# Performance work log

Measured on AMD Instinct MI355X. Metric: run time of the kernel, lower is better.

Reference implementation:

```python
import jax, jax.numpy as jnp
import numpy as np

# TISA RBF basis (helpers l2_dist / rbf_basis in the repo): f_i(d) = a_i * exp(-|b_i| * (d - c_i)^2)

def setup_inputs() -> dict:
    key = jax.random.key(0)
    k = jax.random.split(key, 8)
    B, L, H, D, S, F = 2, 2048, 8, 64, 2, 5
    qs = jax.random.normal(k[0], (B, L, H, D), dtype=jnp.float32)
    ks = jax.random.normal(k[1], (B, L, H, D), dtype=jnp.float32)
    vs = jax.random.normal(k[2], (B, L, H, D), dtype=jnp.float32)
    qs_s = jax.random.uniform(k[3], (B, L, S), dtype=jnp.float32)
    ks_s = jax.random.uniform(k[4], (B, L, S), dtype=jnp.float32)
    a = jax.random.uniform(k[5], (H * F,), dtype=jnp.float32)
    b = jax.random.uniform(k[6], (H * F,), dtype=jnp.float32)
    c = jax.random.normal(k[7], (H * F,), dtype=jnp.float32) * 0.5
    return {"qs": qs, "ks": ks, "vs": vs, "qs_s": qs_s, "ks_s": ks_s, "a": a, "b": b, "c": c}


def _tisa_attention(qs, ks, vs, qs_s, ks_s, a, b, c):
    B, Q, H, D = qs.shape
    F = a.size // H
    aH, bH, cH = (p.reshape(H, F) for p in (a, b, c))
    # pairwise euclidean distance between query and key locations: [B, Q, K]
    diff = qs_s[:, :, None, :] - ks_s[:, None, :, :]
    d = jnp.sqrt(jnp.sum(diff * diff, axis=-1))
    d_ = d[:, None]  # [B, 1, Q, K] broadcast over heads
    # RBF bias summed over F basis functions (small fixed F -> python sum avoids B,H,F,Q,K blowup)
    bias = sum(
        aH[:, f][None, :, None, None]
        * jnp.exp(-jnp.abs(bH[:, f])[None, :, None, None] * (d_ - cH[:, f][None, :, None, None]) ** 2)
        for f in range(F)
    )  # [B, H, Q, K]
    scale = 1.0 / jnp.sqrt(jnp.asarray(D, dtype=qs.dtype))
    scores = jnp.einsum('bqhd,bkhd->bhqk', qs * scale, ks) + bias
    attn = jax.nn.softmax(scores, axis=-1)
    return jnp.einsum('bhqk,bkhd->bqhd', attn, vs)


def reference(qs, ks, vs, qs_s, ks_s, a, b, c):
    # Matches scan_tisa_biased_attention: online-softmax chunking is mathematically
    # identical to a single stable softmax over the full key axis.
    return _tisa_attention(qs, ks, vs, qs_s, ks_s, a, b, c)
```

## Files before the change

### kernel.cpp

```cpp
#include <hip/hip_runtime.h>
#include <cmath>

typedef _Float16 half8 __attribute__((ext_vector_type(8)));
typedef _Float16 half4 __attribute__((ext_vector_type(4)));
typedef _Float16 half2v __attribute__((ext_vector_type(2)));
typedef __fp16 fp16x2 __attribute__((ext_vector_type(2)));
typedef float f32x4 __attribute__((ext_vector_type(4)));
typedef float f32x2 __attribute__((ext_vector_type(2)));

#define B_ 2
#define L_ 2048
#define H_ 8
#define D_ 64
#define S_ 2
#define F_ 5
#define LUTN 2048
#define LSCALE 1448.1547f
#define LOG2E 1.44269504f
#define QSC (0.125f * LOG2E)

#define QOFF 0
#define KOFF 2097152
#define VOFF 4194304
#define SOFFH 6291456
#define WS_NEED 12615680

#define OFF_K0 0
#define OFF_K1 16384
#define OFF_V0 32768
#define OFF_V1 49152
#define OFF_LUT 65536
#define ARENA_SZ 73744
#define SLOTF (16 * 68 + 16)

#define GLOBAL_LOAD_LDS16(g, l)                                                  \
  __builtin_amdgcn_global_load_lds((const __attribute__((address_space(1))) void*)(g), \
                                   (__attribute__((address_space(3))) void*)(l), 16, 0, 0)

#define FAST_SQRT(x) __builtin_amdgcn_sqrtf(x)

#define VTS 68
__global__ __launch_bounds__(512, 8)
void tisa_preproc(const float* __restrict__ qs, const float* __restrict__ ks,
                  const float* __restrict__ vs, const float* __restrict__ ks_s,
                  _Float16* __restrict__ wsh) {
  __shared__ _Float16 VT[64 * VTS];
  const int t = threadIdx.x;
  const int bid = blockIdx.x;
  const int xcd = bid & 7, slot = bid >> 3;
  const int u = slot & 31;
  const int bh = xcd * 2 + (slot >> 5);
  const size_t base = ((size_t)(bh >> 3) * L_ + (size_t)u * 64) * (H_ * D_) + (size_t)(bh & 7) * D_;

  {
    int row = t >> 3, c = t & 7;
    const float* src = qs + base + (size_t)row * 512 + c * 8;
    f32x4 x0 = ((const f32x4*)src)[0], x1 = ((const f32x4*)src)[1];
    half8 hh;
#pragma unroll
    for (int k = 0; k < 4; ++k) { hh[k] = (_Float16)(x0[k] * QSC); hh[k + 4] = (_Float16)(x1[k] * QSC); }
    *(half8*)&wsh[QOFF + ((size_t)bh * 32 + u) * 4096 + row * 64 + (c ^ (row & 7)) * 8] = hh;
  }
  {
    int tile = t >> 8, row = (t >> 3) & 31, c = t & 7;
    const float* src = ks + base + (size_t)(tile * 32 + row) * 512 + c * 8;
    f32x4 x0 = ((const f32x4*)src)[0], x1 = ((const f32x4*)src)[1];
    half8 hh;
#pragma unroll
    for (int k = 0; k < 4; ++k) { hh[k] = (_Float16)x0[k]; hh[k + 4] = (_Float16)x1[k]; }
    *(half8*)&wsh[KOFF + ((size_t)bh * 64 + u * 2 + tile) * 2048 + row * 64 + (c ^ (row & 7)) * 8] = hh;
  }
  if ((bh & 7) == 0 && t < 32) {
    const int b = bh >> 3;
    const float* src = ks_s + ((size_t)b * L_ + u * 64) * 2 + t * 4;
    float* dst = (float*)(wsh + SOFFH) + ((size_t)b * L_ + u * 64) * 2 + t * 4;
    f32x4 x = *(const f32x4*)src;
    x *= LSCALE;
    *(f32x4*)dst = x;
  }
  if (t < 256) {
    int kk = (t & 31) * 2, dg = (t >> 5) * 8;
    const float* s0 = vs + base + (size_t)kk * 512 + dg;
    const float* s1 = s0 + 512;
    f32x4 a0 = ((const f32x4*)s0)[0], a1 = ((const f32x4*)s0)[1];
    f32x4 b0 = ((const f32x4*)s1)[0], b1 = ((const f32x4*)s1)[1];
#pragma unroll
    for (int v = 0; v < 4; ++v) {
      half2v p0 = {(_Float16)a0[v], (_Float16)b0[v]};
      *(half2v*)&VT[(dg + v) * VTS + kk] = p0;
      half2v p1 = {(_Float16)a1[v], (_Float16)b1[v]};
      *(half2v*)&VT[(dg + 4 + v) * VTS + kk] = p1;
    }
  }
  __syncthreads();
  {
    int tile = t >> 8, s = (t >> 3) & 31, cp2 = t & 7;
    int d = 2 * s + (cp2 >> 2), qp = cp2 & 3;
    half4 lo = *(const half4*)&VT[d * VTS + tile * 32 + qp * 4];
    half4 hi = *(const half4*)&VT[d * VTS + tile * 32 + 16 + qp * 4];
    half8 hh;
#pragma unroll
    for (int j = 0; j < 4; ++j) { hh[j] = lo[j]; hh[j + 4] = hi[j]; }
    *(half8*)&wsh[VOFF + ((size_t)bh * 64 + u * 2 + tile) * 2048 + s * 64 + (cp2 ^ (s & 7)) * 8] = hh;
  }
}

__global__ __launch_bounds__(512, 4)
void tisa_attn_main(const float* __restrict__ qs_s, const float* __restrict__ ap,
                    const float* __restrict__ bp, const float* __restrict__ cp,
                    const _Float16* __restrict__ wsh, float* __restrict__ out) {
  __shared__ __align__(16) char arena[ARENA_SZ];
  float* LUT = (float*)(arena + OFF_LUT);

  const int t = threadIdx.x;
  const int lane = t & 63;
  const int w = t >> 6;
  const int g = w >> 1;
  const int qh = w & 1;
  const int tg = t & 127;
  const int quad = lane >> 4;
  const int l16 = lane & 15;

  const int bid = blockIdx.x;
  const int xcd = bid & 7, slot = bid >> 3;
  const int qt = slot & 31;
  const int bh = xcd * 2 + (slot >> 5);
  const int h = bh & 7;
  const int b = bh >> 3;
  const int q0 = qt * 64;

  {
    float af[F_], nb[F_], cf[F_];
#pragma unroll
    for (int f = 0; f < F_; ++f) {
      af[f] = ap[h * F_ + f];
      nb[f] = -fabsf(bp[h * F_ + f]);
      cf[f] = cp[h * F_ + f];
    }
    for (int i = t; i <= LUTN; i += 512) {
      float d = ((float)i + 0.5f) * (1.0f / LSCALE);
      float s = 0.f;
#pragma unroll
      for (int f = 0; f < F_; ++f) {
        float e = d - cf[f];
        s += af[f] * __expf(nb[f] * (e * e));
      }
      LUT[i] = (s - 8.0f) * LOG2E;
    }
  }

  float qx[2], qy[2];
#pragma unroll
  for (int s = 0; s < 2; ++s) {
    qx[s] = qs_s[((size_t)b * L_ + q0 + (qh * 2 + s) * 16 + l16) * 2 + 0] * LSCALE;
    qy[s] = qs_s[((size_t)b * L_ + q0 + (qh * 2 + s) * 16 + l16) * 2 + 1] * LSCALE;
  }

  const _Float16* Qt = wsh + QOFF + ((size_t)bh * 32 + qt) * 4096;
  const _Float16* Kbh = wsh + KOFF + (size_t)bh * 64 * 2048;
  const _Float16* Vbh = wsh + VOFF + (size_t)bh * 64 * 2048;
  const float* wsS = (const float*)(wsh + SOFFH);

  const _Float16* ksrc = Kbh + (size_t)(g * 16) * 2048 + tg * 8;
  const _Float16* vsrc = Vbh + (size_t)(g * 16) * 2048 + tg * 8;
  char* kdst = arena + OFF_K0 + g * 4096 + qh * 1024;
  char* vdst = arena + OFF_V0 + g * 4096 + qh * 1024;
  const float* sbase = wsS + ((size_t)b * L_ + g * 512 + quad * 4) * 2;

  GLOBAL_LOAD_LDS16(Qt + w * 512 + lane * 8, arena + OFF_K1 + w * 1024);
  GLOBAL_LOAD_LDS16(ksrc, kdst);
  GLOBAL_LOAD_LDS16(ksrc + 1024, kdst + 2048);
  GLOBAL_LOAD_LDS16(vsrc, vdst);
  GLOBAL_LOAD_LDS16(vsrc + 1024, vdst + 2048);
  ksrc += 2048; vsrc += 2048;
  __syncthreads();

  half8 qA[2][2];
#pragma unroll
  for (int s = 0; s < 2; ++s)
#pragma unroll
    for (int kb = 0; kb < 2; ++kb)
      qA[s][kb] = *(const half8*)(arena + OFF_K1 + ((qh * 2 + s) * 16 + l16) * 128 +
                                  ((kb * 4 + quad) ^ (l16 & 7)) * 16);
  __syncthreads();

  f32x4 oc[2][4];
#pragma unroll
  for (int s = 0; s < 2; ++s)
#pragma unroll
    for (int df = 0; df < 4; ++df) oc[s][df] = (f32x4){0.f, 0.f, 0.f, 0.f};
  f32x4 lsacc[2];
  lsacc[0] = (f32x4){0.f, 0.f, 0.f, 0.f};
  lsacc[1] = (f32x4){0.f, 0.f, 0.f, 0.f};
  half8 onesv;
#pragma unroll
  for (int j = 0; j < 8; ++j) onesv[j] = (_Float16)1.0f;

  int cur16 = 0;
  for (int it = 0; it < 16; ++it) {
    const int nxt16 = cur16 ^ 16384;
    if (it < 15) {
      GLOBAL_LOAD_LDS16(ksrc, kdst + nxt16);
      GLOBAL_LOAD_LDS16(ksrc + 1024, kdst + nxt16 + 2048);
      GLOBAL_LOAD_LDS16(vsrc, vdst + nxt16);
      GLOBAL_LOAD_LDS16(vsrc + 1024, vdst + nxt16 + 2048);
      ksrc += 2048; vsrc += 2048;
    }

    const float* sit = sbase + it * 64;
    f32x4 cA = *(const f32x4*)(sit);
    f32x4 cB = *(const f32x4*)(sit + 4);
    f32x4 cC = *(const f32x4*)(sit + 32);
    f32x4 cD = *(const f32x4*)(sit + 36);
    float kx[8] = {cA.x, cA.z, cB.x, cB.z, cC.x, cC.z, cD.x, cD.z};
    float ky[8] = {cA.y, cA.w, cB.y, cB.w, cC.y, cC.w, cD.y, cD.w};

    half8 kf[2][2];
#pragma unroll
    for (int nf = 0; nf < 2; ++nf)
#pragma unroll
      for (int kb = 0; kb < 2; ++kb)
        kf[nf][kb] = *(const half8*)(arena + OFF_K0 + cur16 + g * 4096 +
                                     (nf * 16 + l16) * 128 + ((kb * 4 + quad) ^ (l16 & 7)) * 16);
    f32x4 acc[2][2];
#pragma unroll
    for (int s = 0; s < 2; ++s)
#pragma unroll
      for (int nf = 0; nf < 2; ++nf) {
        f32x4 a = (f32x4){0.f, 0.f, 0.f, 0.f};
        a = __builtin_amdgcn_mfma_f32_16x16x32_f16(kf[nf][0], qA[s][0], a, 0, 0, 0);
        a = __builtin_amdgcn_mfma_f32_16x16x32_f16(kf[nf][1], qA[s][1], a, 0, 0, 0);
        acc[s][nf] = a;
      }

    half8 pw[2];
#pragma unroll
    for (int s = 0; s < 2; ++s) {
      float parr[8];
#pragma unroll
      for (int j = 0; j < 8; ++j) {
        float dx = qx[s] - kx[j], dy = qy[s] - ky[j];
        float tt = FAST_SQRT(fmaf(dx, dx, dy * dy));
        parr[j] = __builtin_amdgcn_exp2f(acc[s][j >> 2][j & 3] + LUT[(int)tt]);
      }
      union { half8 h8; fp16x2 h2[4]; } pu;
#pragma unroll
      for (int k = 0; k < 4; ++k)
        pu.h2[k] = __builtin_amdgcn_cvt_pkrtz(parr[2 * k], parr[2 * k + 1]);
      pw[s] = pu.h8;
    }

    lsacc[0] = __builtin_amdgcn_mfma_f32_16x16x32_f16(pw[0], onesv, lsacc[0], 0, 0, 0);
    lsacc[1] = __builtin_amdgcn_mfma_f32_16x16x32_f16(pw[1], onesv, lsacc[1], 0, 0, 0);
#pragma unroll
    for (int df = 0; df < 4; ++df) {
      half8 vf = *(const half8*)(arena + OFF_V0 + cur16 + g * 4096 + (l16 >> 1) * 128 + df * 1024 +
                                 ((((l16 & 1) * 4 + quad) ^ ((l16 >> 1) & 7)) * 16));
      oc[0][df] = __builtin_amdgcn_mfma_f32_16x16x32_f16(pw[0], vf, oc[0][df], 0, 0, 0);
      oc[1][df] = __builtin_amdgcn_mfma_f32_16x16x32_f16(pw[1], vf, oc[1][df], 0, 0, 0);
    }

    __syncthreads();
    cur16 = nxt16;
  }

  float lred[2][4];
#pragma unroll
  for (int s = 0; s < 2; ++s)
#pragma unroll
    for (int r = 0; r < 4; ++r) lred[s][r] = lsacc[s][r];
  __syncthreads();
  float* slots = (float*)arena;
  if (g >= 2) {
#pragma unroll
    for (int s = 0; s < 2; ++s) {
      float* sl = slots + ((g - 2) * 4 + qh * 2 + s) * SLOTF;
#pragma unroll
      for (int df = 0; df < 4; ++df)
#pragma unroll
        for (int r = 0; r < 4; ++r)
          sl[(quad * 4 + r) * 68 + df * 16 + l16] = oc[s][df][r];
      if (l16 == 0) {
#pragma unroll
        for (int r = 0; r < 4; ++r) sl[16 * 68 + quad * 4 + r] = lred[s][r];
      }
    }
  }
  __syncthreads();
  if (g < 2) {
#pragma unroll
    for (int s = 0; s < 2; ++s) {
      float* sl = slots + (g * 4 + qh * 2 + s) * SLOTF;
#pragma unroll
      for (int df = 0; df < 4; ++df)
#pragma unroll
        for (int r = 0; r < 4; ++r)
          oc[s][df][r] += sl[(quad * 4 + r) * 68 + df * 16 + l16];
#pragma unroll
      for (int r = 0; r < 4; ++r) lred[s][r] += sl[16 * 68 + quad * 4 + r];
    }
  }
  if (g == 1) {
#pragma unroll
    for (int s = 0; s < 2; ++s) {
      float* sl = slots + (4 + qh * 2 + s) * SLOTF;
#pragma unroll
      for (int df = 0; df < 4; ++df)
#pragma unroll
        for (int r = 0; r < 4; ++r)
          sl[(quad * 4 + r) * 68 + df * 16 + l16] = oc[s][df][r];
      if (l16 == 0) {
#pragma unroll
        for (int r = 0; r < 4; ++r) sl[16 * 68 + quad * 4 + r] = lred[s][r];
      }
    }
  }
  __syncthreads();
  if (g == 0) {
#pragma unroll
    for (int s = 0; s < 2; ++s) {
      float* sl = slots + (4 + qh * 2 + s) * SLOTF;
      float inv_l[4];
#pragma unroll
      for (int r = 0; r < 4; ++r)
        inv_l[r] = 1.f / (lred[s][r] + sl[16 * 68 + quad * 4 + r]);
#pragma unroll
      for (int df = 0; df < 4; ++df)
#pragma unroll
        for (int r = 0; r < 4; ++r) {
          int qrow = q0 + (qh * 2 + s) * 16 + quad * 4 + r;
          float v = oc[s][df][r] + sl[(quad * 4 + r) * 68 + df * 16 + l16];
          out[((size_t)(b * L_ + qrow)) * (H_ * D_) + h * D_ + df * 16 + l16] = v * inv_l[r];
        }
    }
  }
}

#define KSTR 72
#define PH 72
#define FLUTN 512
#define FLSCALE 362.03867f
__global__ __launch_bounds__(512, 4)
void tisa_attn_fallback(const float* __restrict__ qs, const float* __restrict__ ks,
                        const float* __restrict__ vs, const float* __restrict__ qs_s,
                        const float* __restrict__ ks_s, const float* __restrict__ ap,
                        const float* __restrict__ bp, const float* __restrict__ cp,
                        float* __restrict__ out) {
  __shared__ _Float16 Ks[2][64 * KSTR];
  __shared__ _Float16 VT[2][D_ * KSTR];
  __shared__ _Float16 Pf[8][16 * PH];
  __shared__ float kss2[2][64 * 2];
  __shared__ f32x2 LUT2s[FLUTN + 1];
  __shared__ float comb[4][16][64];
  __shared__ float combl[4][16];

  const int t = threadIdx.x;
  const int lane = t & 63;
  const int w = t >> 6;
  const int g = w >> 2;
  const int qw = w & 3;
  const int t2 = t & 255;
  const int quad = lane >> 4;
  const int l16 = lane & 15;
  const int qt = blockIdx.x & 31;
  const int bh = blockIdx.x >> 5;
  const int h = bh & 7;
  const int b = bh >> 3;
  const int q0 = qt * 64;

  float af[F_], nb[F_], cf[F_];
#pragma unroll
  for (int f = 0; f < F_; ++f) {
    af[f] = ap[h * F_ + f];
    nb[f] = -fabsf(bp[h * F_ + f]);
    cf[f] = cp[h * F_ + f];
  }
  for (int i = t; i <= FLUTN; i += 512) {
    float d0 = (float)i * (1.0f / FLSCALE), d1 = (float)(i + 1) * (1.0f / FLSCALE);
    float s0 = 0.f, s1 = 0.f;
#pragma unroll
    for (int f = 0; f < F_; ++f) {
      float e0 = d0 - cf[f], e1 = d1 - cf[f];
      s0 += af[f] * __expf(nb[f] * (e0 * e0));
      s1 += af[f] * __expf(nb[f] * (e1 * e1));
    }
    LUT2s[i] = (f32x2){s0 - 8.0f, s1 - 8.0f};
  }
  float qx[4], qy[4];
#pragma unroll
  for (int r = 0; r < 4; ++r) {
    int qrow = q0 + qw * 16 + quad * 4 + r;
    qx[r] = qs_s[(b * L_ + qrow) * S_ + 0];
    qy[r] = qs_s[(b * L_ + qrow) * S_ + 1];
  }
  if (t < 256) {
    const int row = t >> 2, dc = (t & 3) * 16;
    const float* src = qs + (((size_t)(b * L_ + q0 + row)) * H_ + h) * D_ + dc;
    const f32x4* s4 = (const f32x4*)src;
    f32x4 v0 = s4[0], v1 = s4[1], v2 = s4[2], v3 = s4[3];
    half8 w0, w1;
#pragma unroll
    for (int u = 0; u < 4; ++u) {
      w0[u] = (_Float16)(v0[u] * 0.125f); w0[u + 4] = (_Float16)(v1[u] * 0.125f);
      w1[u] = (_Float16)(v2[u] * 0.125f); w1[u + 4] = (_Float16)(v3[u] * 0.125f);
    }
    *(half8*)&Ks[0][row * KSTR + dc] = w0;
    *(half8*)&Ks[0][row * KSTR + dc + 8] = w1;
  }
  __syncthreads();
  half8 qA[2];
#pragma unroll
  for (int kb = 0; kb < 2; ++kb)
    qA[kb] = *(const half8*)&Ks[0][(qw * 16 + l16) * KSTR + kb * 32 + quad * 8];
  f32x4 oc[4];
#pragma unroll
  for (int df = 0; df < 4; ++df) oc[df] = (f32x4){0.f, 0.f, 0.f, 0.f};
  float l_r[4] = {0.f, 0.f, 0.f, 0.f};

  for (int it = 0; it < 16; ++it) {
    const int k0 = (g * 16 + it) * 64;
    __syncthreads();
    {
      const int row = t2 >> 2, dc = (t2 & 3) * 16;
      const float* src = ks + (((size_t)(b * L_ + k0 + row)) * H_ + h) * D_ + dc;
      const f32x4* s4 = (const f32x4*)src;
      f32x4 v0 = s4[0], v1 = s4[1], v2 = s4[2], v3 = s4[3];
      half8 w0, w1;
#pragma unroll
      for (int u = 0; u < 4; ++u) {
        w0[u] = (_Float16)v0[u]; w0[u + 4] = (_Float16)v1[u];
        w1[u] = (_Float16)v2[u]; w1[u + 4] = (_Float16)v3[u];
      }
      *(half8*)&Ks[g][row * KSTR + dc] = w0;
      *(half8*)&Ks[g][row * KSTR + dc + 8] = w1;
    }
    {
      const int kk = (t2 & 31) * 2, dg = (t2 >> 5) * 8;
      const float* s0 = vs + (((size_t)(b * L_ + k0 + kk)) * H_ + h) * D_ + dg;
      const float* s1 = s0 + H_ * D_;
      f32x4 a0 = ((const f32x4*)s0)[0], a1 = ((const f32x4*)s0)[1];
      f32x4 b0 = ((const f32x4*)s1)[0], b1 = ((const f32x4*)s1)[1];
#pragma unroll
      for (int u = 0; u < 4; ++u) {
        half2v p0 = {(_Float16)a0[u], (_Float16)b0[u]};
        *(half2v*)&VT[g][(dg + u) * KSTR + kk] = p0;
        half2v p1 = {(_Float16)a1[u], (_Float16)b1[u]};
        *(half2v*)&VT[g][(dg + 4 + u) * KSTR + kk] = p1;
      }
    }
    if (t2 < 128) kss2[g][t2] = ks_s[((size_t)(b * L_) + k0 + (t2 >> 1)) * S_ + (t2 & 1)];
    __syncthreads();
    f32x4 acc[4];
#pragma unroll
    for (int nf = 0; nf < 4; ++nf) {
      f32x4 a = (f32x4){0.f, 0.f, 0.f, 0.f};
#pragma unroll
      for (int kb = 0; kb < 2; ++kb) {
        half8 kf = *(const half8*)&Ks[g][(nf * 16 + l16) * KSTR + kb * 32 + quad * 8];
        a = __builtin_amdgcn_mfma_f32_16x16x32_f16(qA[kb], kf, a, 0, 0, 0);
      }
      acc[nf] = a;
    }
#pragma unroll
    for (int nf = 0; nf < 4; ++nf) {
      float kx = kss2[g][(nf * 16 + l16) * 2 + 0];
      float ky = kss2[g][(nf * 16 + l16) * 2 + 1];
#pragma unroll
      for (int r = 0; r < 4; ++r) {
        float dx = qx[r] - kx, dy = qy[r] - ky;
        float dist = FAST_SQRT(fmaf(dx, dx, dy * dy));
        float tt = dist * FLSCALE;
        int ii = (int)tt;
        float fr = tt - (float)ii;
        f32x2 lh = LUT2s[ii];
        float p = __expf(acc[nf][r] + fmaf(fr, lh.y - lh.x, lh.x));
        acc[nf][r] = p;
      }
    }
#pragma unroll
    for (int r = 0; r < 4; ++r)
      l_r[r] += (acc[0][r] + acc[1][r]) + (acc[2][r] + acc[3][r]);
#pragma unroll
    for (int nf = 0; nf < 4; ++nf)
#pragma unroll
      for (int r = 0; r < 4; ++r)
        Pf[w][(quad * 4 + r) * PH + nf * 16 + l16] = (_Float16)acc[nf][r];
#pragma unroll
    for (int kb = 0; kb < 2; ++kb) {
      half8 pa = *(const half8*)&Pf[w][l16 * PH + kb * 32 + quad * 8];
#pragma unroll
      for (int df = 0; df < 4; ++df) {
        half8 vf = *(const half8*)&VT[g][(df * 16 + l16) * KSTR + kb * 32 + quad * 8];
        oc[df] = __builtin_amdgcn_mfma_f32_16x16x32_f16(pa, vf, oc[df], 0, 0, 0);
      }
    }
  }
  __syncthreads();
  float lred[4];
#pragma unroll
  for (int r = 0; r < 4; ++r) {
    float s = l_r[r];
    s += __shfl_xor(s, 1); s += __shfl_xor(s, 2);
    s += __shfl_xor(s, 4); s += __shfl_xor(s, 8);
    lred[r] = s;
  }
  if (g == 1) {
#pragma unroll
    for (int df = 0; df < 4; ++df)
#pragma unroll
      for (int r = 0; r < 4; ++r)
        comb[qw][quad * 4 + r][df * 16 + l16] = oc[df][r];
    if (l16 == 0) {
#pragma unroll
      for (int r = 0; r < 4; ++r) combl[qw][quad * 4 + r] = lred[r];
    }
  }
  __syncthreads();
  if (g == 0) {
    float inv_l[4];
#pragma unroll
    for (int r = 0; r < 4; ++r)
      inv_l[r] = 1.f / (lred[r] + combl[qw][quad * 4 + r]);
#pragma unroll
    for (int df = 0; df < 4; ++df)
#pragma unroll
      for (int r = 0; r < 4; ++r) {
        int qrow = q0 + qw * 16 + quad * 4 + r;
        float v = oc[df][r] + combl[qw][quad * 4 + r] * 0.f + comb[qw][quad * 4 + r][df * 16 + l16];
        out[(((size_t)(b * L_ + qrow)) * H_ + h) * D_ + df * 16 + l16] = v * inv_l[r];
      }
  }
}

extern "C" void kernel_launch(void* const* d_in, const int* in_sizes, int n_in,
                              void* d_out, int out_size, void* d_ws, size_t ws_size,
                              hipStream_t stream) {
  const float* qs = (const float*)d_in[0];
  const float* ks = (const float*)d_in[1];
  const float* vs = (const float*)d_in[2];
  const float* qs_s = (const float*)d_in[3];
  const float* ks_s = (const float*)d_in[4];
  const float* ap = (const float*)d_in[5];
  const float* bp = (const float*)d_in[6];
  const float* cp = (const float*)d_in[7];
  float* out = (float*)d_out;

  if (ws_size >= (size_t)WS_NEED) {
    _Float16* wsh = (_Float16*)d_ws;
    tisa_preproc<<<dim3(512), dim3(512), 0, stream>>>(qs, ks, vs, ks_s, wsh);
    tisa_attn_main<<<dim3(512), dim3(512), 0, stream>>>(qs_s, ap, bp, cp, wsh, out);
  } else {
    tisa_attn_fallback<<<dim3(512), dim3(512), 0, stream>>>(qs, ks, vs, qs_s, ks_s, ap, bp, cp, out);
  }
}
```

Before: 123.4 us.

## Double attention block to 1024 threads with 8 key groups, drop LDS double buffer

The main attention kernel now launches 1024 threads per block, so eight key groups each handle 256 keys in 8 iterations instead of four groups doing 16. The K/V LDS double buffer is removed: each iteration loads its tile, then synchronises before computing. This relies on the extra waves to hide load latency rather than on prefetching. The cross-group reduction becomes a three-level tree with more barriers, and the tighter launch bounds may raise register pressure.

```diff
diff --git a/kernel.cpp b/kernel.cpp
--- a/kernel.cpp
+++ b/kernel.cpp
@@ -25,10 +25,8 @@
 #define SOFFH 6291456
 #define WS_NEED 12615680
 
-#define OFF_K0 0
-#define OFF_K1 16384
-#define OFF_V0 32768
-#define OFF_V1 49152
+#define OFF_K 0
+#define OFF_V 32768
 #define OFF_LUT 65536
 #define ARENA_SZ 73744
 #define SLOTF (16 * 68 + 16)
@@ -105,7 +103,7 @@
   }
 }
 
-__global__ __launch_bounds__(512, 4)
+__global__ __launch_bounds__(1024, 8)
 void tisa_attn_main(const float* __restrict__ qs_s, const float* __restrict__ ap,
                     const float* __restrict__ bp, const float* __restrict__ cp,
                     const _Float16* __restrict__ wsh, float* __restrict__ out) {
@@ -137,7 +135,7 @@
       nb[f] = -fabsf(bp[h * F_ + f]);
       cf[f] = cp[h * F_ + f];
     }
-    for (int i = t; i <= LUTN; i += 512) {
+    for (int i = t; i <= LUTN; i += 1024) {
       float d = ((float)i + 0.5f) * (1.0f / LSCALE);
       float s = 0.f;
 #pragma unroll
@@ -161,18 +159,14 @@
   const _Float16* Vbh = wsh + VOFF + (size_t)bh * 64 * 2048;
   const float* wsS = (const float*)(wsh + SOFFH);
 
-  const _Float16* ksrc = Kbh + (size_t)(g * 16) * 2048 + tg * 8;
-  const _Float16* vsrc = Vbh + (size_t)(g * 16) * 2048 + tg * 8;
-  char* kdst = arena + OFF_K0 + g * 4096 + qh * 1024;
-  char* vdst = arena + OFF_V0 + g * 4096 + qh * 1024;
-  const float* sbase = wsS + ((size_t)b * L_ + g * 512 + quad * 4) * 2;
-
-  GLOBAL_LOAD_LDS16(Qt + w * 512 + lane * 8, arena + OFF_K1 + w * 1024);
-  GLOBAL_LOAD_LDS16(ksrc, kdst);
-  GLOBAL_LOAD_LDS16(ksrc + 1024, kdst + 2048);
-  GLOBAL_LOAD_LDS16(vsrc, vdst);
-  GLOBAL_LOAD_LDS16(vsrc + 1024, vdst + 2048);
-  ksrc += 2048; vsrc += 2048;
+  const _Float16* ksrc = Kbh + (size_t)(g * 8) * 2048 + tg * 8;
+  const _Float16* vsrc = Vbh + (size_t)(g * 8) * 2048 + tg * 8;
+  char* kdst = arena + OFF_K + g * 4096 + qh * 1024;
+  char* vdst = arena + OFF_V + g * 4096 + qh * 1024;
+  const float* sbase = wsS + ((size_t)b * L_ + g * 256 + quad * 4) * 2;
+
+  if (w < 8)
+    GLOBAL_LOAD_LDS16(Qt + w * 512 + lane * 8, arena + OFF_K + w * 1024);
   __syncthreads();
 
   half8 qA[2][2];
@@ -180,7 +174,7 @@
   for (int s = 0; s < 2; ++s)
 #pragma unroll
     for (int kb = 0; kb < 2; ++kb)
-      qA[s][kb] = *(const half8*)(arena + OFF_K1 + ((qh * 2 + s) * 16 + l16) * 128 +
+      qA[s][kb] = *(const half8*)(arena + OFF_K + ((qh * 2 + s) * 16 + l16) * 128 +
                                   ((kb * 4 + quad) ^ (l16 & 7)) * 16);
   __syncthreads();
 
@@ -196,16 +190,13 @@
 #pragma unroll
   for (int j = 0; j < 8; ++j) onesv[j] = (_Float16)1.0f;
 
-  int cur16 = 0;
-  for (int it = 0; it < 16; ++it) {
-    const int nxt16 = cur16 ^ 16384;
-    if (it < 15) {
-      GLOBAL_LOAD_LDS16(ksrc, kdst + nxt16);
-      GLOBAL_LOAD_LDS16(ksrc + 1024, kdst + nxt16 + 2048);
-      GLOBAL_LOAD_LDS16(vsrc, vdst + nxt16);
-      GLOBAL_LOAD_LDS16(vsrc + 1024, vdst + nxt16 + 2048);
-      ksrc += 2048; vsrc += 2048;
-    }
+  for (int it = 0; it < 8; ++it) {
+    GLOBAL_LOAD_LDS16(ksrc, kdst);
+    GLOBAL_LOAD_LDS16(ksrc + 1024, kdst + 2048);
+    GLOBAL_LOAD_LDS16(vsrc, vdst);
+    GLOBAL_LOAD_LDS16(vsrc + 1024, vdst + 2048);
+    ksrc += 2048; vsrc += 2048;
+    __syncthreads();
 
     const float* sit = sbase + it * 64;
     f32x4 cA = *(const f32x4*)(sit);
@@ -220,7 +211,7 @@
     for (int nf = 0; nf < 2; ++nf)
 #pragma unroll
       for (int kb = 0; kb < 2; ++kb)
-        kf[nf][kb] = *(const half8*)(arena + OFF_K0 + cur16 + g * 4096 +
+        kf[nf][kb] = *(const half8*)(arena + OFF_K + g * 4096 +
                                      (nf * 16 + l16) * 128 + ((kb * 4 + quad) ^ (l16 & 7)) * 16);
     f32x4 acc[2][2];
 #pragma unroll
@@ -254,14 +245,13 @@
     lsacc[1] = __builtin_amdgcn_mfma_f32_16x16x32_f16(pw[1], onesv, lsacc[1], 0, 0, 0);
 #pragma unroll
     for (int df = 0; df < 4; ++df) {
-      half8 vf = *(const half8*)(arena + OFF_V0 + cur16 + g * 4096 + (l16 >> 1) * 128 + df * 1024 +
+      half8 vf = *(const half8*)(arena + OFF_V + g * 4096 + (l16 >> 1) * 128 + df * 1024 +
                                  ((((l16 & 1) * 4 + quad) ^ ((l16 >> 1) & 7)) * 16));
       oc[0][df] = __builtin_amdgcn_mfma_f32_16x16x32_f16(pw[0], vf, oc[0][df], 0, 0, 0);
       oc[1][df] = __builtin_amdgcn_mfma_f32_16x16x32_f16(pw[1], vf, oc[1][df], 0, 0, 0);
     }
 
     __syncthreads();
-    cur16 = nxt16;
   }
 
   float lred[2][4];
@@ -269,12 +259,12 @@
   for (int s = 0; s < 2; ++s)
 #pragma unroll
     for (int r = 0; r < 4; ++r) lred[s][r] = lsacc[s][r];
-  __syncthreads();
   float* slots = (float*)arena;
-  if (g >= 2) {
-#pragma unroll
-    for (int s = 0; s < 2; ++s) {
-      float* sl = slots + ((g - 2) * 4 + qh * 2 + s) * SLOTF;
+
+  if (g >= 4) {
+#pragma unroll
+    for (int s = 0; s < 2; ++s) {
+      float* sl = slots + ((g - 4) * 4 + qh * 2 + s) * SLOTF;
 #pragma unroll
       for (int df = 0; df < 4; ++df)
 #pragma unroll
@@ -287,7 +277,7 @@
     }
   }
   __syncthreads();
-  if (g < 2) {
+  if (g < 4) {
 #pragma unroll
     for (int s = 0; s < 2; ++s) {
       float* sl = slots + (g * 4 + qh * 2 + s) * SLOTF;
@@ -300,10 +290,11 @@
       for (int r = 0; r < 4; ++r) lred[s][r] += sl[16 * 68 + quad * 4 + r];
     }
   }
-  if (g == 1) {
-#pragma unroll
-    for (int s = 0; s < 2; ++s) {
-      float* sl = slots + (4 + qh * 2 + s) * SLOTF;
+  __syncthreads();
+  if (g == 2 || g == 3) {
+#pragma unroll
+    for (int s = 0; s < 2; ++s) {
+      float* sl = slots + ((g - 2) * 4 + qh * 2 + s) * SLOTF;
 #pragma unroll
       for (int df = 0; df < 4; ++df)
 #pragma unroll
@@ -316,10 +307,40 @@
     }
   }
   __syncthreads();
+  if (g < 2) {
+#pragma unroll
+    for (int s = 0; s < 2; ++s) {
+      float* sl = slots + (g * 4 + qh * 2 + s) * SLOTF;
+#pragma unroll
+      for (int df = 0; df < 4; ++df)
+#pragma unroll
+        for (int r = 0; r < 4; ++r)
+          oc[s][df][r] += sl[(quad * 4 + r) * 68 + df * 16 + l16];
+#pragma unroll
+      for (int r = 0; r < 4; ++r) lred[s][r] += sl[16 * 68 + quad * 4 + r];
+    }
+  }
+  __syncthreads();
+  if (g == 1) {
+#pragma unroll
+    for (int s = 0; s < 2; ++s) {
+      float* sl = slots + (qh * 2 + s) * SLOTF;
+#pragma unroll
+      for (int df = 0; df < 4; ++df)
+#pragma unroll
+        for (int r = 0; r < 4; ++r)
+          sl[(quad * 4 + r) * 68 + df * 16 + l16] = oc[s][df][r];
+      if (l16 == 0) {
+#pragma unroll
+        for (int r = 0; r < 4; ++r) sl[16 * 68 + quad * 4 + r] = lred[s][r];
+      }
+    }
+  }
+  __syncthreads();
   if (g == 0) {
 #pragma unroll
     for (int s = 0; s < 2; ++s) {
-      float* sl = slots + (4 + qh * 2 + s) * SLOTF;
+      float* sl = slots + (qh * 2 + s) * SLOTF;
       float inv_l[4];
 #pragma unroll
       for (int r = 0; r < 4; ++r)
@@ -548,7 +569,7 @@
   if (ws_size >= (size_t)WS_NEED) {
     _Float16* wsh = (_Float16*)d_ws;
     tisa_preproc<<<dim3(512), dim3(512), 0, stream>>>(qs, ks, vs, ks_s, wsh);
-    tisa_attn_main<<<dim3(512), dim3(512), 0, stream>>>(qs_s, ap, bp, cp, wsh, out);
+    tisa_attn_main<<<dim3(512), dim3(1024), 0, stream>>>(qs_s, ap, bp, cp, wsh, out);
   } else {
     tisa_attn_fallback<<<dim3(512), dim3(512), 0, stream>>>(qs, ks, vs, qs_s, ks_s, ap, bp, cp, out);
   }
```

Measured after the change: 357.2 us. 189% more time.

## Drop K/V double buffering to halve LDS arena and raise occupancy

Applied to the files above, without the earlier changes.

Replaces the double-buffered K/V LDS staging with a single buffer that is loaded at the top of each iteration and followed by a barrier, so loads no longer overlap compute. This roughly halves the shared-memory arena, which lets more workgroups reside per CU and hide latency through occupancy instead of software prefetch. The LUT shrinks by one entry and the distance index is clamped so it stays in range. The trade-off is exposed global-to-LDS latency on every iteration inside each workgroup.

```diff
diff --git a/kernel.cpp b/kernel.cpp
--- a/kernel.cpp
+++ b/kernel.cpp
@@ -25,12 +25,10 @@
 #define SOFFH 6291456
 #define WS_NEED 12615680
 
-#define OFF_K0 0
-#define OFF_K1 16384
-#define OFF_V0 32768
-#define OFF_V1 49152
-#define OFF_LUT 65536
-#define ARENA_SZ 73744
+#define OFF_K 0
+#define OFF_V 16384
+#define OFF_LUT 32768
+#define ARENA_SZ 40960
 #define SLOTF (16 * 68 + 16)
 
 #define GLOBAL_LOAD_LDS16(g, l)                                                  \
@@ -137,7 +135,7 @@
       nb[f] = -fabsf(bp[h * F_ + f]);
       cf[f] = cp[h * F_ + f];
     }
-    for (int i = t; i <= LUTN; i += 512) {
+    for (int i = t; i < LUTN; i += 512) {
       float d = ((float)i + 0.5f) * (1.0f / LSCALE);
       float s = 0.f;
 #pragma unroll
@@ -163,16 +161,11 @@
 
   const _Float16* ksrc = Kbh + (size_t)(g * 16) * 2048 + tg * 8;
   const _Float16* vsrc = Vbh + (size_t)(g * 16) * 2048 + tg * 8;
-  char* kdst = arena + OFF_K0 + g * 4096 + qh * 1024;
-  char* vdst = arena + OFF_V0 + g * 4096 + qh * 1024;
+  char* kdst = arena + OFF_K + g * 4096 + qh * 1024;
+  char* vdst = arena + OFF_V + g * 4096 + qh * 1024;
   const float* sbase = wsS + ((size_t)b * L_ + g * 512 + quad * 4) * 2;
 
-  GLOBAL_LOAD_LDS16(Qt + w * 512 + lane * 8, arena + OFF_K1 + w * 1024);
-  GLOBAL_LOAD_LDS16(ksrc, kdst);
-  GLOBAL_LOAD_LDS16(ksrc + 1024, kdst + 2048);
-  GLOBAL_LOAD_LDS16(vsrc, vdst);
-  GLOBAL_LOAD_LDS16(vsrc + 1024, vdst + 2048);
-  ksrc += 2048; vsrc += 2048;
+  GLOBAL_LOAD_LDS16(Qt + w * 512 + lane * 8, arena + OFF_K + w * 1024);
   __syncthreads();
 
   half8 qA[2][2];
@@ -180,7 +173,7 @@
   for (int s = 0; s < 2; ++s)
 #pragma unroll
     for (int kb = 0; kb < 2; ++kb)
-      qA[s][kb] = *(const half8*)(arena + OFF_K1 + ((qh * 2 + s) * 16 + l16) * 128 +
+      qA[s][kb] = *(const half8*)(arena + OFF_K + ((qh * 2 + s) * 16 + l16) * 128 +
                                   ((kb * 4 + quad) ^ (l16 & 7)) * 16);
   __syncthreads();
 
@@ -196,16 +189,13 @@
 #pragma unroll
   for (int j = 0; j < 8; ++j) onesv[j] = (_Float16)1.0f;
 
-  int cur16 = 0;
   for (int it = 0; it < 16; ++it) {
-    const int nxt16 = cur16 ^ 16384;
-    if (it < 15) {
-      GLOBAL_LOAD_LDS16(ksrc, kdst + nxt16);
-      GLOBAL_LOAD_LDS16(ksrc + 1024, kdst + nxt16 + 2048);
-      GLOBAL_LOAD_LDS16(vsrc, vdst + nxt16);
-      GLOBAL_LOAD_LDS16(vsrc + 1024, vdst + nxt16 + 2048);
-      ksrc += 2048; vsrc += 2048;
-    }
+    GLOBAL_LOAD_LDS16(ksrc, kdst);
+    GLOBAL_LOAD_LDS16(ksrc + 1024, kdst + 2048);
+    GLOBAL_LOAD_LDS16(vsrc, vdst);
+    GLOBAL_LOAD_LDS16(vsrc + 1024, vdst + 2048);
+    ksrc += 2048; vsrc += 2048;
+    __syncthreads();
 
     const float* sit = sbase + it * 64;
     f32x4 cA = *(const f32x4*)(sit);
@@ -220,7 +210,7 @@
     for (int nf = 0; nf < 2; ++nf)
 #pragma unroll
       for (int kb = 0; kb < 2; ++kb)
-        kf[nf][kb] = *(const half8*)(arena + OFF_K0 + cur16 + g * 4096 +
+        kf[nf][kb] = *(const half8*)(arena + OFF_K + g * 4096 +
                                      (nf * 16 + l16) * 128 + ((kb * 4 + quad) ^ (l16 & 7)) * 16);
     f32x4 acc[2][2];
 #pragma unroll
@@ -240,7 +230,7 @@
 #pragma unroll
       for (int j = 0; j < 8; ++j) {
         float dx = qx[s] - kx[j], dy = qy[s] - ky[j];
-        float tt = FAST_SQRT(fmaf(dx, dx, dy * dy));
+        float tt = fminf(FAST_SQRT(fmaf(dx, dx, dy * dy)), 2047.0f);
         parr[j] = __builtin_amdgcn_exp2f(acc[s][j >> 2][j & 3] + LUT[(int)tt]);
       }
       union { half8 h8; fp16x2 h2[4]; } pu;
@@ -254,14 +244,13 @@
     lsacc[1] = __builtin_amdgcn_mfma_f32_16x16x32_f16(pw[1], onesv, lsacc[1], 0, 0, 0);
 #pragma unroll
     for (int df = 0; df < 4; ++df) {
-      half8 vf = *(const half8*)(arena + OFF_V0 + cur16 + g * 4096 + (l16 >> 1) * 128 + df * 1024 +
+      half8 vf = *(const half8*)(arena + OFF_V + g * 4096 + (l16 >> 1) * 128 + df * 1024 +
                                  ((((l16 & 1) * 4 + quad) ^ ((l16 >> 1) & 7)) * 16));
       oc[0][df] = __builtin_amdgcn_mfma_f32_16x16x32_f16(pw[0], vf, oc[0][df], 0, 0, 0);
       oc[1][df] = __builtin_amdgcn_mfma_f32_16x16x32_f16(pw[1], vf, oc[1][df], 0, 0, 0);
     }
 
     __syncthreads();
-    cur16 = nxt16;
   }
 
   float lred[2][4];
@@ -269,7 +258,6 @@
   for (int s = 0; s < 2; ++s)
 #pragma unroll
     for (int r = 0; r < 4; ++r) lred[s][r] = lsacc[s][r];
-  __syncthreads();
   float* slots = (float*)arena;
   if (g >= 2) {
 #pragma unroll
```

Result: slower. 128.3 us (+3.9%).
